# Kernel optimization log

Hardware: AMD Instinct MI355X
Metric: run time of the kernel (lower is better)

Reference implementation:

```python
import jax, jax.numpy as jnp
import numpy as np
from jax import lax

DN = ('NCHW', 'OIHW', 'NCHW')

def _conv(x, w, b):
    y = lax.conv_general_dilated(x, w, (1, 1), 'SAME', dimension_numbers=DN)
    return y + b[None, :, None, None]

def setup_inputs() -> dict:
    key = jax.random.key(0)
    ks = jax.random.split(key, 12)
    B, C, H, W = 8, 32, 128, 128
    Cb, INT, K, FK = 64, 64, 3, 3
    inp = {
        'z': jax.random.normal(ks[0], (B, C, H, W), jnp.float32),
        'backbone': jax.random.normal(ks[1], (B, Cb, H, W), jnp.float32),
        'mem_stab': jax.random.normal(ks[2], (B, C, H, W), jnp.float32),
        'mem_unstab': jax.random.normal(ks[3], (B, C, H, W), jnp.float32),
        'w0': jax.random.normal(ks[4], (INT, Cb + 3 * C, K, K), jnp.float32) * 0.05,
        'b0': jnp.zeros((INT,), jnp.float32),
        'w1': jax.random.normal(ks[5], (INT, INT, K, K), jnp.float32) * 0.05,
        'b1': jnp.zeros((INT,), jnp.float32),
        'w2': jax.random.normal(ks[6], (INT, INT, K, K), jnp.float32) * 0.05,
        'b2': jnp.zeros((INT,), jnp.float32),
        'w_last': jax.random.normal(ks[7], (C * FK * FK, INT, K, K), jnp.float32) * 0.05,
        'b_last': jnp.full((C * FK * FK,), -4.0, jnp.float32),
        'fusion_kernel_size': FK,
    }
    return inp

def reference(z, backbone, mem_stab, mem_unstab, w0, b0, w1, b1, w2, b2, w_last, b_last, fusion_kernel_size):
    B, C, H, W = z.shape
    k = int(fusion_kernel_size)
    p = k * k
    # controller conv stack (LeakyReLU slope 0.01, matching nn.LeakyReLU default)
    q = jnp.concatenate([backbone, z, mem_stab, mem_unstab], axis=1)
    q = jax.nn.leaky_relu(_conv(q, w0, b0), 0.01)
    q = jax.nn.leaky_relu(_conv(q, w1, b1), 0.01)
    q = jax.nn.leaky_relu(_conv(q, w2, b2), 0.01)
    # fusion head -> [B, C, p, HW]
    head = _conv(q, w_last, b_last).reshape(B, C, p, H * W)
    # softmax over p kernel positions + one extra logit-0 slot for z itself
    eta = jax.nn.softmax(jnp.concatenate([head, jnp.zeros_like(head[:, :, :1])], axis=2), axis=2)
    # unfold(mem_stab, k, padding=k//2): patches ordered (c, kh, kw) like torch unfold
    pad = k // 2
    mpad = jnp.pad(mem_stab, ((0, 0), (0, 0), (pad, pad), (pad, pad)))
    patches = jnp.stack([mpad[:, :, i:i + H, j:j + W] for i in range(k) for j in range(k)], axis=2)
    patches = patches.reshape(B, C, p, H * W)
    z_flat = z.reshape(B, C, H * W)
    z_stab = (patches * eta[:, :, :p]).sum(axis=2) + eta[:, :, p] * z_flat
    return z_stab.reshape(B, C, H, W)
```

## Files before the change

### kernel.cpp

```cpp
#include <hip/hip_runtime.h>
#include <hip/hip_fp16.h>

typedef _Float16 half8 __attribute__((ext_vector_type(8)));
typedef _Float16 half4v __attribute__((ext_vector_type(4)));
typedef float floatx4 __attribute__((ext_vector_type(4)));

#define HW 128
#define IMG (HW * HW)
#define PH 130
#define WP 200
#define XP 164

typedef __attribute__((address_space(3))) _Float16 lds_f16;
typedef __attribute__((address_space(1))) const _Float16 glb_f16;
__device__ __forceinline__ void gload16(const _Float16* g, _Float16* l) {
    __builtin_amdgcn_global_load_lds((glb_f16*)g, (lds_f16*)l, 16, 0, 0);
}

__global__ void pack_w_all(const float* __restrict__ w0, const float* __restrict__ w1,
                           const float* __restrict__ w2, const float* __restrict__ wl,
                           _Float16* __restrict__ p0, _Float16* __restrict__ p1,
                           _Float16* __restrict__ p2, _Float16* __restrict__ pl) {
    int idx = blockIdx.x * 256 + threadIdx.x;
    if (idx < 92160) {
        int local = idx;
        int o = local / 1440;
        int rem = local % 1440;
        int c = rem / 9;
        int t = rem % 9;
        int oh = o >> 5, n = (o >> 4) & 1, l15 = o & 15;
        int cb = c >> 5, l4 = (c >> 3) & 3, e = c & 7;
        int frag = (t * 5 + cb) * 2 + n;
        p0[(size_t)oh * 46080 + frag * 512 + (l4 * 16 + l15) * 8 + e] =
            (_Float16)w0[local];
        return;
    }
    const float* w; _Float16* p; int C; int local;
    if (idx < 129024)      { w = w1; p = p1; C = 64;  local = idx - 92160; }
    else if (idx < 165888) { w = w2; p = p2; C = 64;  local = idx - 129024; }
    else if (idx < 331776) { w = wl; p = pl; C = 64;  local = idx - 165888; }
    else return;
    int o = local / (C * 9);
    int rem = local % (C * 9);
    int c = rem / 9;
    int t = rem % 9;
    p[(o * 9 + t) * C + c] = (_Float16)w[local];
}

__device__ __forceinline__ void zero_halo(_Float16* P, int C, int id) {
    int nvec = C / 8;
    int b = id / (516 * nvec);
    int r = id % (516 * nvec);
    int cell = r / nvec;
    int v = r % nvec;
    int hh, ww;
    if (cell < 130)      { hh = 0;   ww = cell; }
    else if (cell < 260) { hh = 129; ww = cell - 130; }
    else if (cell < 388) { hh = cell - 260 + 1; ww = 0; }
    else                 { hh = cell - 388 + 1; ww = 129; }
    half8 z8 = {};
    *reinterpret_cast<half8*>(P + (((size_t)b * PH + hh) * PH + ww) * C + v * 8) = z8;
}

__global__ void zero_pads_pre(_Float16* __restrict__ X0, _Float16* __restrict__ Q1) {
    int id = blockIdx.x * 256 + threadIdx.x;
    if (id < 82560) zero_halo(X0, 160, id);
    else if (id < 115584) zero_halo(Q1, 64, id - 82560);
}

__global__ void zero_pads64(_Float16* __restrict__ P) {
    int id = blockIdx.x * 256 + threadIdx.x;
    if (id < 33024) zero_halo(P, 64, id);
}

__global__ __launch_bounds__(256)
void pack_in(const float* __restrict__ z, const float* __restrict__ bb,
             const float* __restrict__ ms, const float* __restrict__ mu,
             _Float16* __restrict__ X0) {
    __shared__ _Float16 lds[160 * 132];
    int b = blockIdx.x >> 7;
    int h = blockIdx.x & 127;
    int tid = threadIdx.x;

    for (int i = 0; i < 20; i++) {
        int id = i * 256 + tid;
        int c = id >> 5;
        int col = (id & 31) * 4;
        const float* src; int cs; int csz;
        if (c < 64)       { src = bb; cs = c;       csz = 64; }
        else if (c < 96)  { src = z;  cs = c - 64;  csz = 32; }
        else if (c < 128) { src = ms; cs = c - 96;  csz = 32; }
        else              { src = mu; cs = c - 128; csz = 32; }
        float4 v = *reinterpret_cast<const float4*>(
            src + ((size_t)b * csz + cs) * IMG + h * HW + col);
        half4v hv = { (_Float16)v.x, (_Float16)v.y, (_Float16)v.z, (_Float16)v.w };
        *reinterpret_cast<half4v*>(&lds[c * 132 + col]) = hv;
    }
    __syncthreads();
    _Float16* dst = X0 + (((size_t)b * PH + (h + 1)) * PH + 1) * 160;
    for (int i = 0; i < 10; i++) {
        int id = i * 256 + tid;
        int pix = id / 20;
        int c0 = (id % 20) * 8;
        half8 hv;
        #pragma unroll
        for (int e = 0; e < 8; e++) hv[e] = lds[(c0 + e) * 132 + pix];
        *reinterpret_cast<half8*>(dst + (size_t)pix * 160 + c0) = hv;
    }
}

__global__ __launch_bounds__(256, 2)
void conv3_c160(const _Float16* __restrict__ X, const _Float16* __restrict__ Wp,
                const float* __restrict__ bias, _Float16* __restrict__ Y) {
    __shared__ _Float16 xs[130 * XP];
    int b = blockIdx.x >> 7;
    int h = blockIdx.x & 127;
    int tid = threadIdx.x;
    int lane = tid & 63;
    int wave = tid >> 6;
    int ph = wave & 1;
    int oh = wave >> 1;
    int l15 = lane & 15;
    int l4  = lane >> 4;

    floatx4 acc[4][2] = {};
    half8 SA[10], SB[10];

    const _Float16* wl = Wp + (size_t)oh * 46080 + lane * 8;

#define LOADW(S, k) { \
    _Pragma("unroll") \
    for (int cb = 0; cb < 5; cb++) \
      _Pragma("unroll") \
      for (int n = 0; n < 2; n++) \
        S[cb * 2 + n] = *reinterpret_cast<const half8*>( \
            wl + (size_t)(((k) * 5 + cb) * 2 + n) * 512); }

#define STAGE160(r) { \
    const _Float16* grow = X + ((size_t)b * PH + (h + (r))) * PH * 160; \
    _Pragma("unroll") \
    for (int i = 0; i < 11; i++) { \
      int id = i * 256 + tid; \
      if (id < 2600) { \
        half8 v = *reinterpret_cast<const half8*>(grow + (size_t)id * 8); \
        *reinterpret_cast<half8*>(&xs[(id / 20) * XP + (id % 20) * 8]) = v; \
      } } }

#define COMP160(dw, S) { \
    _Pragma("unroll") \
    for (int cb = 0; cb < 5; cb++) { \
      int kofs = cb * 32 + l4 * 8; \
      half8 af[4]; \
      _Pragma("unroll") \
      for (int m = 0; m < 4; m++) { \
        int p = ph * 64 + m * 16 + l15; \
        af[m] = *reinterpret_cast<const half8*>(&xs[(p + (dw)) * XP + kofs]); \
      } \
      _Pragma("unroll") \
      for (int m = 0; m < 4; m++) \
        _Pragma("unroll") \
        for (int n = 0; n < 2; n++) \
          acc[m][n] = __builtin_amdgcn_mfma_f32_16x16x32_f16( \
              af[m], S[cb * 2 + n], acc[m][n], 0, 0, 0); } }

    LOADW(SA, 0);
    STAGE160(0);
    __syncthreads();
    LOADW(SB, 1);  COMP160(0, SA);
    LOADW(SA, 2);  COMP160(1, SB);
    LOADW(SB, 3);  COMP160(2, SA);
    __syncthreads();
    STAGE160(1);
    __syncthreads();
    LOADW(SA, 4);  COMP160(0, SB);
    LOADW(SB, 5);  COMP160(1, SA);
    LOADW(SA, 6);  COMP160(2, SB);
    __syncthreads();
    STAGE160(2);
    __syncthreads();
    LOADW(SB, 7);  COMP160(0, SA);
    LOADW(SA, 8);  COMP160(1, SB);
    COMP160(2, SA);

#undef LOADW
#undef STAGE160
#undef COMP160

    _Float16* dst = Y + (((size_t)b * PH + (h + 1)) * PH + 1) * 64;
    #pragma unroll
    for (int m = 0; m < 4; m++)
        #pragma unroll
        for (int n = 0; n < 2; n++) {
            int o = oh * 32 + n * 16 + l15;
            float bv = bias[o];
            #pragma unroll
            for (int q = 0; q < 4; q++) {
                int pix = ph * 64 + m * 16 + l4 * 4 + q;
                float v = acc[m][n][q] + bv;
                v = v > 0.f ? v : 0.01f * v;
                dst[(size_t)pix * 64 + o] = (_Float16)v;
            }
        }
}

__global__ __launch_bounds__(256, 3)
void conv3_c64(const _Float16* __restrict__ X, const _Float16* __restrict__ Wp,
               const float* __restrict__ bias, _Float16* __restrict__ Y) {
    __shared__ _Float16 smem[9360 + 64 * WP];
    _Float16* xs = smem;
    _Float16* wbuf = smem + 9360;
    int b = blockIdx.x >> 7;
    int h = blockIdx.x & 127;
    int tid = threadIdx.x;
    int lane = tid & 63;
    int wave = tid >> 6;
    int ph = wave & 1;
    int oh = wave >> 1;
    int l15 = lane & 15;
    int l4  = lane >> 4;

    floatx4 acc[4][2] = {};
    const _Float16* xbase = X + ((size_t)b * PH + h) * (PH * 64);

    for (int r = 0; r < 3; r++) {
        if (r) __syncthreads();
        for (int i = 0; i < 5; i++) {
            int id = i * 256 + tid;
            if (id < 1040) {
                half8 v = *reinterpret_cast<const half8*>(
                    xbase + (size_t)r * (PH * 64) + (size_t)id * 8);
                *reinterpret_cast<half8*>(&xs[(id >> 3) * 72 + (id & 7) * 8]) = v;
            }
        }
        for (int i = 0; i < 6; i++) {
            int id = i * 256 + tid;
            int o = id / 24, j = id % 24;
            half8 v = *reinterpret_cast<const half8*>(
                Wp + ((size_t)o * 9 + r * 3) * 64 + j * 8);
            *reinterpret_cast<half8*>(&wbuf[o * WP + j * 8]) = v;
        }
        __syncthreads();
        #pragma unroll
        for (int dw = 0; dw < 3; dw++)
            #pragma unroll
            for (int cb = 0; cb < 2; cb++) {
                int kofs = cb * 32 + l4 * 8;
                half8 bf[2];
                #pragma unroll
                for (int n = 0; n < 2; n++) {
                    int o = oh * 32 + n * 16 + l15;
                    bf[n] = *reinterpret_cast<const half8*>(
                        &wbuf[o * WP + dw * 64 + kofs]);
                }
                half8 af[4];
                #pragma unroll
                for (int m = 0; m < 4; m++) {
                    int p = ph * 64 + m * 16 + l15;
                    af[m] = *reinterpret_cast<const half8*>(&xs[(p + dw) * 72 + kofs]);
                }
                #pragma unroll
                for (int m = 0; m < 4; m++)
                    #pragma unroll
                    for (int n = 0; n < 2; n++)
                        acc[m][n] = __builtin_amdgcn_mfma_f32_16x16x32_f16(
                            af[m], bf[n], acc[m][n], 0, 0, 0);
            }
    }
    _Float16* dst = Y + (((size_t)b * PH + (h + 1)) * PH + 1) * 64;
    #pragma unroll
    for (int m = 0; m < 4; m++)
        #pragma unroll
        for (int n = 0; n < 2; n++) {
            int o = oh * 32 + n * 16 + l15;
            float bv = bias[o];
            #pragma unroll
            for (int q = 0; q < 4; q++) {
                int pix = ph * 64 + m * 16 + l4 * 4 + q;
                float v = acc[m][n][q] + bv;
                v = v > 0.f ? v : 0.01f * v;
                dst[(size_t)pix * 64 + o] = (_Float16)v;
            }
        }
}

__global__ __launch_bounds__(256, 3)
void head_gemm(const _Float16* __restrict__ X, const _Float16* __restrict__ Wp,
               const float* __restrict__ b_last, _Float16* __restrict__ Lg,
               int bbase) {
    __shared__ _Float16 smem[26752];
    _Float16* xs = smem;
    _Float16* wbuf = smem + 8320;
    _Float16* tb = smem;
    int blk = blockIdx.x;
    int ct = blk >> 9;
    int bi = (blk >> 7) & 3;
    int h  = blk & 127;
    int b = bbase + bi;
    int tid = threadIdx.x;
    int lane = tid & 63;
    int wave = tid >> 6;
    int pxh = wave & 1;
    int og  = wave >> 1;
    int l15 = lane & 15;
    int l4  = lane >> 4;

    floatx4 acc[4][3] = {};
    const _Float16* xbase = X + ((size_t)b * PH + h) * (PH * 64);
    const _Float16* wbase = Wp + (size_t)ct * 96 * 9 * 64;

    for (int r = 0; r < 3; r++) {
        if (r) __syncthreads();
        const _Float16* xrow = xbase + (size_t)r * (PH * 64);
        for (int i = 0; i < 5; i++) {
            int sbase = i * 256 + wave * 64;
            int s = sbase + lane;
            if (s < 1040) {
                int px = s >> 3;
                int j = (s & 7) ^ (px & 7);
                gload16(xrow + (size_t)(px * 8 + j) * 8, xs + (size_t)sbase * 8);
            }
        }
        const _Float16* wrow = wbase + r * 192;
        for (int i = 0; i < 9; i++) {
            int tbs = i * 256 + wave * 64;
            int t = tbs + lane;
            int o = t / 24, ks = t % 24;
            int k = (ks & 0x18) | ((ks & 7) ^ (o & 7));
            gload16(wrow + (size_t)(o * 576 + k * 8), wbuf + (size_t)tbs * 8);
        }
        __syncthreads();
        #pragma unroll
        for (int dw = 0; dw < 3; dw++)
            #pragma unroll
            for (int cb = 0; cb < 2; cb++) {
                int kb = dw * 8 + cb * 4 + l4;
                half8 bf[3];
                #pragma unroll
                for (int n = 0; n < 3; n++) {
                    int ol = og * 48 + n * 16 + l15;
                    int ksw = (kb & 0x18) | ((kb & 7) ^ (ol & 7));
                    bf[n] = *reinterpret_cast<const half8*>(&wbuf[ol * 192 + ksw * 8]);
                }
                int j = cb * 4 + l4;
                half8 af[4];
                #pragma unroll
                for (int m = 0; m < 4; m++) {
                    int px = pxh * 64 + m * 16 + l15 + dw;
                    af[m] = *reinterpret_cast<const half8*>(
                        &xs[px * 64 + (j ^ (px & 7)) * 8]);
                }
                #pragma unroll
                for (int m = 0; m < 4; m++)
                    #pragma unroll
                    for (int n = 0; n < 3; n++)
                        acc[m][n] = __builtin_amdgcn_mfma_f32_16x16x32_f16(
                            af[m], bf[n], acc[m][n], 0, 0, 0);
            }
    }
    __syncthreads();

    #pragma unroll
    for (int m = 0; m < 4; m++)
        #pragma unroll
        for (int n = 0; n < 3; n++) {
            int od = og * 48 + n * 16 + l15;
            float bv = b_last[ct * 96 + od];
            half4v hv;
            #pragma unroll
            for (int q = 0; q < 4; q++) hv[q] = (_Float16)(acc[m][n][q] + bv);
            *reinterpret_cast<half4v*>(&tb[od * 132 + pxh * 64 + m * 16 + l4 * 4]) = hv;
        }
    __syncthreads();

    _Float16* dst = Lg + (((size_t)bi * 128 + h) * 288 + (size_t)ct * 96) * 128;
    #pragma unroll
    for (int i = 0; i < 6; i++) {
        int id = i * 256 + tid;
        int od = id >> 4;
        int sl = id & 15;
        half8 v = *reinterpret_cast<const half8*>(&tb[od * 132 + sl * 8]);
        *reinterpret_cast<half8*>(dst + (size_t)od * 128 + sl * 8) = v;
    }
}

__global__ __launch_bounds__(256)
void fuse_sm(const _Float16* __restrict__ Lg, const float* __restrict__ ms,
             const float* __restrict__ zin, float* __restrict__ out, int bbase) {
    int blk = blockIdx.x;
    int bi = blk >> 11;
    int c  = (blk >> 6) & 31;
    int hp = blk & 63;
    int tid = threadIdx.x;
    int h = hp * 2 + (tid >> 7);
    int w = tid & 127;
    int b = bbase + bi;

    const _Float16* lrow = Lg + (((size_t)bi * 128 + h) * 288 + (size_t)c * 9) * 128 + w;
    float L[9];
    float mx = 0.f;
    #pragma unroll
    for (int j = 0; j < 9; j++) { L[j] = (float)lrow[j * 128]; mx = fmaxf(mx, L[j]); }
    float ez = __expf(-mx);
    float sum = ez;
    float e[9];
    #pragma unroll
    for (int j = 0; j < 9; j++) { e[j] = __expf(L[j] - mx); sum += e[j]; }
    float inv = 1.f / sum;
    const float* msb = ms + ((size_t)b * 32 + c) * IMG;
    float accv = ez * inv * zin[((size_t)b * 32 + c) * IMG + h * HW + w];
    #pragma unroll
    for (int kh = 0; kh < 3; kh++) {
        int h2 = h + kh - 1;
        int h2c = min(max(h2, 0), 127);
        bool okh = (unsigned)h2 < 128u;
        #pragma unroll
        for (int kw = 0; kw < 3; kw++) {
            int w2 = w + kw - 1;
            int w2c = min(max(w2, 0), 127);
            bool okw = (unsigned)w2 < 128u;
            float mv = msb[h2c * HW + w2c];
            accv += e[kh * 3 + kw] * inv * ((okh && okw) ? mv : 0.f);
        }
    }
    out[((size_t)b * 32 + c) * IMG + h * HW + w] = accv;
}

extern "C" void kernel_launch(void* const* d_in, const int* in_sizes, int n_in,
                              void* d_out, int out_size, void* d_ws, size_t ws_size,
                              hipStream_t stream) {
    const float* z  = (const float*)d_in[0];
    const float* bb = (const float*)d_in[1];
    const float* ms = (const float*)d_in[2];
    const float* mu = (const float*)d_in[3];
    const float* w0 = (const float*)d_in[4];
    const float* b0 = (const float*)d_in[5];
    const float* w1 = (const float*)d_in[6];
    const float* b1 = (const float*)d_in[7];
    const float* w2 = (const float*)d_in[8];
    const float* b2 = (const float*)d_in[9];
    const float* wl = (const float*)d_in[10];
    const float* bl = (const float*)d_in[11];

    char* ws = (char*)d_ws;
    _Float16* Wp0 = (_Float16*)(ws + 0);
    _Float16* Wp1 = (_Float16*)(ws + 184320);
    _Float16* Wp2 = (_Float16*)(ws + 258048);
    _Float16* WpL = (_Float16*)(ws + 331776);
    _Float16* BufA = (_Float16*)(ws + 663552);
    _Float16* BufB = (_Float16*)(ws + 43927552);

    _Float16* X0 = BufA;
    _Float16* Q1 = BufB;
    _Float16* Q2 = BufA;
    _Float16* Q3 = BufB;
    _Float16* Lg = BufA;

    pack_w_all<<<(331776 + 255) / 256, 256, 0, stream>>>(w0, w1, w2, wl, Wp0, Wp1, Wp2, WpL);
    zero_pads_pre<<<(115584 + 255) / 256, 256, 0, stream>>>(X0, Q1);
    pack_in<<<1024, 256, 0, stream>>>(z, bb, ms, mu, X0);

    conv3_c160<<<1024, 256, 0, stream>>>(X0, Wp0, b0, Q1);
    zero_pads64<<<(33024 + 255) / 256, 256, 0, stream>>>(Q2);
    conv3_c64<<<1024, 256, 0, stream>>>(Q1, Wp1, b1, Q2);
    conv3_c64<<<1024, 256, 0, stream>>>(Q2, Wp2, b2, Q3);

    head_gemm<<<1536, 256, 0, stream>>>(Q3, WpL, bl, Lg, 0);
    fuse_sm<<<8192, 256, 0, stream>>>(Lg, ms, z, (float*)d_out, 0);
    head_gemm<<<1536, 256, 0, stream>>>(Q3, WpL, bl, Lg, 4);
    fuse_sm<<<8192, 256, 0, stream>>>(Lg, ms, z, (float*)d_out, 4);
}
```

Measured before the change: 190.5 us.

## Compute two output rows per block in first conv to reuse staged input rows

The first conv kernel now launches 512-thread blocks that each produce two adjacent output rows. Four input rows are staged into LDS and shared between two wave groups, instead of three rows staged per output row. This reduces global reads and staging work per output. In exchange, each wave group sits idle for one of the four phases, and the tighter launch bounds may pressure registers.

```diff
diff --git a/kernel.cpp b/kernel.cpp
--- a/kernel.cpp
+++ b/kernel.cpp
@@ -109,17 +109,18 @@
     }
 }
 
-__global__ __launch_bounds__(256, 2)
+__global__ __launch_bounds__(512, 4)
 void conv3_c160(const _Float16* __restrict__ X, const _Float16* __restrict__ Wp,
                 const float* __restrict__ bias, _Float16* __restrict__ Y) {
     __shared__ _Float16 xs[130 * XP];
-    int b = blockIdx.x >> 7;
-    int h = blockIdx.x & 127;
+    int b = blockIdx.x >> 6;
+    int h0 = (blockIdx.x & 63) * 2;
     int tid = threadIdx.x;
     int lane = tid & 63;
     int wave = tid >> 6;
+    int rg = wave >> 2;
     int ph = wave & 1;
-    int oh = wave >> 1;
+    int oh = (wave >> 1) & 1;
     int l15 = lane & 15;
     int l4  = lane >> 4;
 
@@ -136,11 +137,11 @@
         S[cb * 2 + n] = *reinterpret_cast<const half8*>( \
             wl + (size_t)(((k) * 5 + cb) * 2 + n) * 512); }
 
-#define STAGE160(r) { \
-    const _Float16* grow = X + ((size_t)b * PH + (h + (r))) * PH * 160; \
+#define STAGE160(g) { \
+    const _Float16* grow = X + ((size_t)b * PH + (h0 + (g))) * PH * 160; \
     _Pragma("unroll") \
-    for (int i = 0; i < 11; i++) { \
-      int id = i * 256 + tid; \
+    for (int i = 0; i < 6; i++) { \
+      int id = i * 512 + tid; \
       if (id < 2600) { \
         half8 v = *reinterpret_cast<const half8*>(grow + (size_t)id * 8); \
         *reinterpret_cast<half8*>(&xs[(id / 20) * XP + (id % 20) * 8]) = v; \
@@ -166,27 +167,51 @@
     LOADW(SA, 0);
     STAGE160(0);
     __syncthreads();
-    LOADW(SB, 1);  COMP160(0, SA);
-    LOADW(SA, 2);  COMP160(1, SB);
-    LOADW(SB, 3);  COMP160(2, SA);
+    if (rg == 0) {
+        LOADW(SB, 1);  COMP160(0, SA);
+        LOADW(SA, 2);  COMP160(1, SB);
+        LOADW(SB, 3);  COMP160(2, SA);
+    } else {
+        LOADW(SB, 1);
+    }
     __syncthreads();
     STAGE160(1);
     __syncthreads();
-    LOADW(SA, 4);  COMP160(0, SB);
-    LOADW(SB, 5);  COMP160(1, SA);
-    LOADW(SA, 6);  COMP160(2, SB);
+    if (rg == 0) {
+        LOADW(SA, 4);  COMP160(0, SB);
+        LOADW(SB, 5);  COMP160(1, SA);
+        LOADW(SA, 6);  COMP160(2, SB);
+    } else {
+        COMP160(0, SA);  LOADW(SA, 2);
+        COMP160(1, SB);  LOADW(SB, 3);
+        COMP160(2, SA);
+    }
     __syncthreads();
     STAGE160(2);
     __syncthreads();
-    LOADW(SB, 7);  COMP160(0, SA);
-    LOADW(SA, 8);  COMP160(1, SB);
-    COMP160(2, SA);
+    if (rg == 0) {
+        LOADW(SB, 7);  COMP160(0, SA);
+        LOADW(SA, 8);  COMP160(1, SB);
+        COMP160(2, SA);
+    } else {
+        LOADW(SA, 4);  COMP160(0, SB);
+        LOADW(SB, 5);  COMP160(1, SA);
+        LOADW(SA, 6);  COMP160(2, SB);
+    }
+    __syncthreads();
+    STAGE160(3);
+    __syncthreads();
+    if (rg == 1) {
+        LOADW(SB, 7);  COMP160(0, SA);
+        LOADW(SA, 8);  COMP160(1, SB);
+        COMP160(2, SA);
+    }
 
 #undef LOADW
 #undef STAGE160
 #undef COMP160
 
-    _Float16* dst = Y + (((size_t)b * PH + (h + 1)) * PH + 1) * 64;
+    _Float16* dst = Y + (((size_t)b * PH + (h0 + rg + 1)) * PH + 1) * 64;
     #pragma unroll
     for (int m = 0; m < 4; m++)
         #pragma unroll
@@ -459,7 +484,7 @@
     zero_pads_pre<<<(115584 + 255) / 256, 256, 0, stream>>>(X0, Q1);
     pack_in<<<1024, 256, 0, stream>>>(z, bb, ms, mu, X0);
 
-    conv3_c160<<<1024, 256, 0, stream>>>(X0, Wp0, b0, Q1);
+    conv3_c160<<<512, 512, 0, stream>>>(X0, Wp0, b0, Q1);
     zero_pads64<<<(33024 + 255) / 256, 256, 0, stream>>>(Q2);
     conv3_c64<<<1024, 256, 0, stream>>>(Q1, Wp1, b1, Q2);
     conv3_c64<<<1024, 256, 0, stream>>>(Q2, Wp2, b2, Q3);
```

Result: slower. 221.2 us (+16.2%).
